# Optimization experiments

Measured on AMD Instinct MI355X. Metric: run time of the kernel, lower is better.

The kernel has to match this reference:

```python
import jax, jax.numpy as jnp
import numpy as np

N_ITER = 9      # n_iter in entmax_nsect_cuda(X, alpha=1.5, n_iter=9, n_sections=4)
N_SECTIONS = 4  # quaternary section search


def _entmax15_nsect(X):
    """1.5-entmax via n-section threshold search.

    p = [(alpha-1)*x - tau]_+^(1/(alpha-1)) with alpha=1.5 -> p = relu(x/2 - tau)^2,
    tau chosen so sum_j p_j = 1. tau lies in [max(x/2)-1, max(x/2)]; the interval is
    narrowed by N_SECTIONS-section search for N_ITER iterations (f is decreasing in tau).
    """
    Xs = X * 0.5
    mx = jnp.max(Xs, axis=-1, keepdims=True)      # (n, 1)
    lo = mx - 1.0
    hi = mx

    def f(tau):  # sum relu(x - tau)^2 - 1, decreasing in tau; (n, 1)
        return jnp.sum(jnp.square(jnp.maximum(Xs - tau, 0.0)), axis=-1, keepdims=True) - 1.0

    for _ in range(N_ITER):
        width = (hi - lo) / N_SECTIONS
        # count of interior grid points with f >= 0 gives the bracketing section index
        count = jnp.zeros_like(lo)
        for j in range(1, N_SECTIONS):
            count = count + (f(lo + j * width) >= 0.0).astype(Xs.dtype)
        lo = lo + width * count
        hi = lo + width

    tau = 0.5 * (lo + hi)
    p = jnp.square(jnp.maximum(Xs - tau, 0.0))
    return p / jnp.sum(p, axis=-1, keepdims=True)  # exact renormalization of approx projection


def setup_inputs() -> dict:
    key = jax.random.key(0)
    kx, kt = jax.random.split(key)
    n, c = 4096, 32000
    X = jax.random.normal(kx, (n, c), dtype=jnp.float32)
    target = jax.random.randint(kt, (n,), 0, c, dtype=jnp.int64)
    return {"X": X, "target": target}


def reference(X, target):
    n = X.shape[0]
    p = _entmax15_nsect(X)                                   # (n, C) simplex projection
    # omega (Tsallis entropy term for alpha=1.5): (1 - sum p^{1.5}) / 0.75
    omega = (1.0 - jnp.sum(p * jnp.sqrt(p), axis=-1)) / 0.75
    # p_star <- p - e_target  (scatter_add_ of -1 at the target column)
    p_star = p.at[jnp.arange(n), target].add(-1.0)
    loss = omega + jnp.sum(p_star * X, axis=-1)              # + einsum('ij,ij->i', p_star, X)
    # ignore_index = -100 < 0 -> no masking; reduction = 'elementwise_mean'
    return jnp.sum(loss) / n
```

## Files before the change

### kernel.cpp

```cpp
#include <hip/hip_runtime.h>


#define NITER 9
#define TGRAW 1.5f
#define CAPW  320
#define EXCAP 3072
#define NW    16

__device__ __forceinline__ float wave_max_f(float m) {
    #pragma unroll
    for (int off = 32; off > 0; off >>= 1) m = fmaxf(m, __shfl_xor(m, off));
    return m;
}
__device__ __forceinline__ float wave_sum_f(float s) {
    #pragma unroll
    for (int off = 32; off > 0; off >>= 1) s += __shfl_xor(s, off);
    return s;
}

__global__ __launch_bounds__(1024, 8)
void entmax_loss_kernel(const float* __restrict__ X,
                        const int* __restrict__ target,
                        float* __restrict__ row_loss, int c) {
    const int r    = blockIdx.x;
    const int tid  = threadIdx.x;
    const int w    = tid >> 6;
    const int lane = tid & 63;
    const float* __restrict__ Xr = X + (size_t)r * (size_t)c;

    __shared__ float seg[NW][CAPW];
    __shared__ int   segcnt[NW];
    __shared__ float s_red[NW];
    __shared__ int   s_excnt[NW];
    __shared__ float ex[EXCAP];
    __shared__ float s_r3[3][NW];
    __shared__ int   s_flag;
    __shared__ int   s_tg;
    __shared__ float s_xtg;

    if (tid == 0) {
        s_flag = 0;
        const int tg = target[r];
        s_tg = tg;
        s_xtg = Xr[tg];
    }

    const int c4 = c >> 2;
    const unsigned long long lt = (1ull << lane) - 1ull;
    float* __restrict__ segw = seg[w];
    float m = -3e38f;
    int   cnt = 0;
    for (int b = 0; b < 2; ++b) {
        float4 v[4];
        #pragma unroll
        for (int k = 0; k < 4; ++k) {
            const int i4 = tid + (b * 4 + k) * 1024;
            if (i4 < c4) v[k] = ((const float4*)Xr)[i4];
            else { v[k].x = v[k].y = v[k].z = v[k].w = -3e38f; }
        }
        #pragma unroll
        for (int k = 0; k < 4; ++k) {
            m = fmaxf(m, fmaxf(fmaxf(v[k].x, v[k].y), fmaxf(v[k].z, v[k].w)));
            const float e[4] = {v[k].x, v[k].y, v[k].z, v[k].w};
            #pragma unroll
            for (int j = 0; j < 4; ++j) {
                const bool p = e[j] > TGRAW;
                const unsigned long long bl = __ballot(p);
                const int pos = cnt + (int)__popcll(bl & lt);
                if (p && pos < CAPW) segw[pos] = e[j];
                cnt += (int)__popcll(bl);
            }
        }
    }
    m = wave_max_f(m);
    if (lane == 0) {
        s_red[w] = m;
        segcnt[w] = cnt;
        if (cnt > CAPW) s_flag = 1;
    }
    __syncthreads();

    float rm = s_red[0];
    #pragma unroll
    for (int i = 1; i < NW; ++i) rm = fmaxf(rm, s_red[i]);
    const bool fb = (s_flag != 0) || (rm < TGRAW + 2.0f);

    if (!fb) {
        const float thr = rm - 2.0f;
        const int sc = segcnt[w];
        int ec = 0;
        for (int i0 = 0; i0 < sc; i0 += 64) {
            const int i = i0 + lane;
            const bool p = (i < sc) && (segw[i] > thr);
            ec += (int)__popcll(__ballot(p));
        }
        if (lane == 0) s_excnt[w] = ec;
        __syncthreads();

        int off = 0, total = 0;
        #pragma unroll
        for (int u = 0; u < NW; ++u) {
            const int e = s_excnt[u];
            if (u < w) off += e;
            total += e;
        }
        if (total <= EXCAP) {
            int pos = off;
            for (int i0 = 0; i0 < sc; i0 += 64) {
                const int i = i0 + lane;
                const bool p = (i < sc) && (segw[i] > thr);
                const unsigned long long bl = __ballot(p);
                if (p) ex[pos + (int)__popcll(bl & lt)] = 0.5f * segw[i];
                pos += (int)__popcll(bl);
            }
            __syncthreads();
            if (w == 0) {
                float lo = 0.5f * rm - 1.0f, hi = 0.5f * rm;
                for (int it = 0; it < NITER; ++it) {
                    const float w4 = (hi - lo) * 0.25f;
                    const float t1 = lo + w4, t2 = lo + 2.f * w4, t3 = lo + 3.f * w4;
                    float f1 = 0.f, f2 = 0.f, f3 = 0.f;
                    for (int i = lane; i < total; i += 64) {
                        const float x = ex[i];
                        float d;
                        d = fmaxf(x - t1, 0.f); f1 = fmaf(d, d, f1);
                        d = fmaxf(x - t2, 0.f); f2 = fmaf(d, d, f2);
                        d = fmaxf(x - t3, 0.f); f3 = fmaf(d, d, f3);
                    }
                    f1 = wave_sum_f(f1); f2 = wave_sum_f(f2); f3 = wave_sum_f(f3);
                    const int cc = (f1 >= 1.f) + (f2 >= 1.f) + (f3 >= 1.f);
                    lo += w4 * (float)cc;
                    hi = lo + w4;
                }
                const float tau = 0.5f * (lo + hi);
                float S1 = 0.f, SX = 0.f, S3 = 0.f;
                for (int i = lane; i < total; i += 64) {
                    const float x = ex[i];
                    const float d = fmaxf(x - tau, 0.f), q = d * d;
                    S1 += q; SX = fmaf(q, x, SX); S3 = fmaf(q, d, S3);
                }
                S1 = wave_sum_f(S1); SX = wave_sum_f(SX); S3 = wave_sum_f(S3);
                if (lane == 0) {
                    const float omega = (1.f - S3 / (S1 * sqrtf(S1))) * (4.f / 3.f);
                    row_loss[r] = omega + 2.f * SX / S1 - s_xtg;
                }
            }
            return;
        }
    }

    {
        float lo = 0.5f * rm - 1.0f, hi = 0.5f * rm;
        for (int it = 0; it < NITER; ++it) {
            const float w4 = (hi - lo) * 0.25f;
            const float t1 = lo + w4, t2 = lo + 2.f * w4, t3 = lo + 3.f * w4;
            float f1 = 0.f, f2 = 0.f, f3 = 0.f;
            for (int i = tid; i < c; i += 1024) {
                const float x = 0.5f * Xr[i];
                float d;
                d = fmaxf(x - t1, 0.f); f1 = fmaf(d, d, f1);
                d = fmaxf(x - t2, 0.f); f2 = fmaf(d, d, f2);
                d = fmaxf(x - t3, 0.f); f3 = fmaf(d, d, f3);
            }
            f1 = wave_sum_f(f1); f2 = wave_sum_f(f2); f3 = wave_sum_f(f3);
            __syncthreads();
            if (lane == 0) { s_r3[0][w] = f1; s_r3[1][w] = f2; s_r3[2][w] = f3; }
            __syncthreads();
            float a = 0.f, bb = 0.f, g = 0.f;
            #pragma unroll
            for (int u = 0; u < NW; ++u) { a += s_r3[0][u]; bb += s_r3[1][u]; g += s_r3[2][u]; }
            const int cc = (a >= 1.f) + (bb >= 1.f) + (g >= 1.f);
            lo += w4 * (float)cc;
            hi = lo + w4;
        }
        const float tau = 0.5f * (lo + hi);
        float S1 = 0.f, SX = 0.f, S3 = 0.f;
        for (int i = tid; i < c; i += 1024) {
            const float x = 0.5f * Xr[i];
            const float d = fmaxf(x - tau, 0.f), q = d * d;
            S1 += q; SX = fmaf(q, x, SX); S3 = fmaf(q, d, S3);
        }
        S1 = wave_sum_f(S1); SX = wave_sum_f(SX); S3 = wave_sum_f(S3);
        __syncthreads();
        if (lane == 0) { s_r3[0][w] = S1; s_r3[1][w] = SX; s_r3[2][w] = S3; }
        __syncthreads();
        if (tid == 0) {
            float a = 0.f, bb = 0.f, g = 0.f;
            #pragma unroll
            for (int u = 0; u < NW; ++u) { a += s_r3[0][u]; bb += s_r3[1][u]; g += s_r3[2][u]; }
            const float omega = (1.f - g / (a * sqrtf(a))) * (4.f / 3.f);
            row_loss[r] = omega + 2.f * bb / a - s_xtg;
        }
    }
}

__global__ __launch_bounds__(256, 4)
void fallback_kernel(const float* __restrict__ X, const int* __restrict__ target,
                     float* __restrict__ row_loss, int n, int c) {
    const int wv   = threadIdx.x >> 6;
    const int lane = threadIdx.x & 63;
    const int r = blockIdx.x * 4 + wv;
    if (r >= n) return;
    const float* __restrict__ Xr = X + (size_t)r * (size_t)c;
    float m = -3e38f;
    for (int i = lane; i < c; i += 64) m = fmaxf(m, Xr[i]);
    m = wave_max_f(m);
    float lo = 0.5f * m - 1.0f, hi = 0.5f * m;
    for (int it = 0; it < NITER; ++it) {
        const float w4 = (hi - lo) * 0.25f;
        const float t1 = lo + w4, t2 = lo + 2.f * w4, t3 = lo + 3.f * w4;
        float f1 = 0.f, f2 = 0.f, f3 = 0.f;
        for (int i = lane; i < c; i += 64) {
            const float x = 0.5f * Xr[i];
            float d;
            d = fmaxf(x - t1, 0.f); f1 = fmaf(d, d, f1);
            d = fmaxf(x - t2, 0.f); f2 = fmaf(d, d, f2);
            d = fmaxf(x - t3, 0.f); f3 = fmaf(d, d, f3);
        }
        f1 = wave_sum_f(f1); f2 = wave_sum_f(f2); f3 = wave_sum_f(f3);
        const int cc = (f1 >= 1.f) + (f2 >= 1.f) + (f3 >= 1.f);
        lo += w4 * (float)cc;
        hi = lo + w4;
    }
    const float tau = 0.5f * (lo + hi);
    float S1 = 0.f, SX = 0.f, S3 = 0.f;
    for (int i = lane; i < c; i += 64) {
        const float x = 0.5f * Xr[i];
        const float d = fmaxf(x - tau, 0.f), q = d * d;
        S1 += q; SX = fmaf(q, x, SX); S3 = fmaf(q, d, S3);
    }
    S1 = wave_sum_f(S1); SX = wave_sum_f(SX); S3 = wave_sum_f(S3);
    if (lane == 0) {
        const float omega = (1.f - S3 / (S1 * sqrtf(S1))) * (4.f / 3.f);
        row_loss[r] = omega + 2.f * SX / S1 - Xr[target[r]];
    }
}

__global__ __launch_bounds__(1024)
void reduce_mean_kernel(const float* __restrict__ vv, float* __restrict__ out, int n) {
    __shared__ float s_red[16];
    float s = 0.f;
    for (int i = threadIdx.x; i < n; i += 1024) s += vv[i];
    s = wave_sum_f(s);
    const int wv = threadIdx.x >> 6;
    const int lane = threadIdx.x & 63;
    if (lane == 0) s_red[wv] = s;
    __syncthreads();
    if (threadIdx.x == 0) {
        float t = 0.f;
        for (int i = 0; i < 16; ++i) t += s_red[i];
        out[0] = t / (float)n;
    }
}

extern "C" void kernel_launch(void* const* d_in, const int* in_sizes, int n_in,
                              void* d_out, int out_size, void* d_ws, size_t ws_size,
                              hipStream_t stream) {
    (void)n_in; (void)out_size;
    const float* X      = (const float*)d_in[0];
    const int*   target = (const int*)d_in[1];
    float*       out    = (float*)d_out;
    float*       row_loss = (float*)d_ws;

    const int n = in_sizes[1];
    const int c = in_sizes[0] / n;

    const bool fast = ((c & 3) == 0) && (c <= 32768) &&
                      (ws_size >= (size_t)n * sizeof(float));
    if (fast) {
        entmax_loss_kernel<<<n, 1024, 0, stream>>>(X, target, row_loss, c);
    } else {
        fallback_kernel<<<(n + 3) / 4, 256, 0, stream>>>(X, target, row_loss, n, c);
    }
    reduce_mean_kernel<<<1, 1024, 0, stream>>>(row_loss, out, n);
}
```

Baseline: 162.5 us.

## Halve block size, prefetch row chunks, and spread threshold search across all waves

The row kernel drops from 1024 to 512 threads per row. Each thread now covers four chunks of float4 loads, and the next chunk is register-prefetched while the current one is filtered, which overlaps memory latency with the ballot compaction. The n-section search over the compacted candidates previously ran on wave 0 alone and now runs on all 8 waves. A double-buffered shared partial array keeps it to one barrier per iteration. The per-wave candidate capacity grows to 512 so the larger per-wave slice does not overflow. This adds barriers and register pressure in exchange for fewer idle waves and better latency hiding.

```diff
diff --git a/kernel.cpp b/kernel.cpp
--- a/kernel.cpp
+++ b/kernel.cpp
@@ -2,10 +2,11 @@
 
 
 #define NITER 9
+#define NTHR  512
+#define NWAVE 8
 #define TGRAW 1.5f
-#define CAPW  320
+#define CAPW  512
 #define EXCAP 3072
-#define NW    16
 
 __device__ __forceinline__ float wave_max_f(float m) {
     #pragma unroll
@@ -18,7 +19,7 @@
     return s;
 }
 
-__global__ __launch_bounds__(1024, 8)
+__global__ __launch_bounds__(NTHR, 8)
 void entmax_loss_kernel(const float* __restrict__ X,
                         const int* __restrict__ target,
                         float* __restrict__ row_loss, int c) {
@@ -28,40 +29,45 @@
     const int lane = tid & 63;
     const float* __restrict__ Xr = X + (size_t)r * (size_t)c;
 
-    __shared__ float seg[NW][CAPW];
-    __shared__ int   segcnt[NW];
-    __shared__ float s_red[NW];
-    __shared__ int   s_excnt[NW];
+    __shared__ float seg[NWAVE][CAPW];
+    __shared__ int   segcnt[NWAVE];
+    __shared__ float s_red[NWAVE];
+    __shared__ int   s_excnt[NWAVE];
     __shared__ float ex[EXCAP];
-    __shared__ float s_r3[3][NW];
+    __shared__ float s_part[2][3][NWAVE];
+    __shared__ float s_fin[3][NWAVE];
     __shared__ int   s_flag;
-    __shared__ int   s_tg;
     __shared__ float s_xtg;
 
-    if (tid == 0) {
-        s_flag = 0;
-        const int tg = target[r];
-        s_tg = tg;
-        s_xtg = Xr[tg];
-    }
+    if (tid == 0) { s_flag = 0; s_xtg = Xr[target[r]]; }
 
     const int c4 = c >> 2;
     const unsigned long long lt = (1ull << lane) - 1ull;
     float* __restrict__ segw = seg[w];
     float m = -3e38f;
     int   cnt = 0;
-    for (int b = 0; b < 2; ++b) {
-        float4 v[4];
+
+    float4 cur[4], nxt[4];
+    #pragma unroll
+    for (int k = 0; k < 4; ++k) {
+        const int i4 = tid + k * NTHR;
+        if (i4 < c4) cur[k] = ((const float4*)Xr)[i4];
+        else { cur[k].x = cur[k].y = cur[k].z = cur[k].w = -3e38f; }
+    }
+    #pragma unroll
+    for (int b = 0; b < 4; ++b) {
+        if (b < 3) {
+            #pragma unroll
+            for (int k = 0; k < 4; ++k) {
+                const int i4 = tid + ((b + 1) * 4 + k) * NTHR;
+                if (i4 < c4) nxt[k] = ((const float4*)Xr)[i4];
+                else { nxt[k].x = nxt[k].y = nxt[k].z = nxt[k].w = -3e38f; }
+            }
+        }
         #pragma unroll
         for (int k = 0; k < 4; ++k) {
-            const int i4 = tid + (b * 4 + k) * 1024;
-            if (i4 < c4) v[k] = ((const float4*)Xr)[i4];
-            else { v[k].x = v[k].y = v[k].z = v[k].w = -3e38f; }
-        }
-        #pragma unroll
-        for (int k = 0; k < 4; ++k) {
-            m = fmaxf(m, fmaxf(fmaxf(v[k].x, v[k].y), fmaxf(v[k].z, v[k].w)));
-            const float e[4] = {v[k].x, v[k].y, v[k].z, v[k].w};
+            const float e[4] = {cur[k].x, cur[k].y, cur[k].z, cur[k].w};
+            m = fmaxf(m, fmaxf(fmaxf(e[0], e[1]), fmaxf(e[2], e[3])));
             #pragma unroll
             for (int j = 0; j < 4; ++j) {
                 const bool p = e[j] > TGRAW;
@@ -71,6 +77,10 @@
                 cnt += (int)__popcll(bl);
             }
         }
+        if (b < 3) {
+            #pragma unroll
+            for (int k = 0; k < 4; ++k) cur[k] = nxt[k];
+        }
     }
     m = wave_max_f(m);
     if (lane == 0) {
@@ -82,7 +92,7 @@
 
     float rm = s_red[0];
     #pragma unroll
-    for (int i = 1; i < NW; ++i) rm = fmaxf(rm, s_red[i]);
+    for (int i = 1; i < NWAVE; ++i) rm = fmaxf(rm, s_red[i]);
     const bool fb = (s_flag != 0) || (rm < TGRAW + 2.0f);
 
     if (!fb) {
@@ -99,7 +109,7 @@
 
         int off = 0, total = 0;
         #pragma unroll
-        for (int u = 0; u < NW; ++u) {
+        for (int u = 0; u < NWAVE; ++u) {
             const int e = s_excnt[u];
             if (u < w) off += e;
             total += e;
@@ -114,36 +124,51 @@
                 pos += (int)__popcll(bl);
             }
             __syncthreads();
-            if (w == 0) {
-                float lo = 0.5f * rm - 1.0f, hi = 0.5f * rm;
-                for (int it = 0; it < NITER; ++it) {
-                    const float w4 = (hi - lo) * 0.25f;
-                    const float t1 = lo + w4, t2 = lo + 2.f * w4, t3 = lo + 3.f * w4;
-                    float f1 = 0.f, f2 = 0.f, f3 = 0.f;
-                    for (int i = lane; i < total; i += 64) {
-                        const float x = ex[i];
-                        float d;
-                        d = fmaxf(x - t1, 0.f); f1 = fmaf(d, d, f1);
-                        d = fmaxf(x - t2, 0.f); f2 = fmaf(d, d, f2);
-                        d = fmaxf(x - t3, 0.f); f3 = fmaf(d, d, f3);
-                    }
-                    f1 = wave_sum_f(f1); f2 = wave_sum_f(f2); f3 = wave_sum_f(f3);
-                    const int cc = (f1 >= 1.f) + (f2 >= 1.f) + (f3 >= 1.f);
-                    lo += w4 * (float)cc;
-                    hi = lo + w4;
+            float lo = 0.5f * rm - 1.0f, hi = 0.5f * rm;
+            for (int it = 0; it < NITER; ++it) {
+                const float w4 = (hi - lo) * 0.25f;
+                const float t1 = lo + w4, t2 = lo + 2.f * w4, t3 = lo + 3.f * w4;
+                float f1 = 0.f, f2 = 0.f, f3 = 0.f;
+                for (int i = tid; i < total; i += NTHR) {
+                    const float x = ex[i];
+                    float d;
+                    d = fmaxf(x - t1, 0.f); f1 = fmaf(d, d, f1);
+                    d = fmaxf(x - t2, 0.f); f2 = fmaf(d, d, f2);
+                    d = fmaxf(x - t3, 0.f); f3 = fmaf(d, d, f3);
                 }
-                const float tau = 0.5f * (lo + hi);
-                float S1 = 0.f, SX = 0.f, S3 = 0.f;
-                for (int i = lane; i < total; i += 64) {
-                    const float x = ex[i];
-                    const float d = fmaxf(x - tau, 0.f), q = d * d;
-                    S1 += q; SX = fmaf(q, x, SX); S3 = fmaf(q, d, S3);
+                f1 = wave_sum_f(f1); f2 = wave_sum_f(f2); f3 = wave_sum_f(f3);
+                const int pb = it & 1;
+                if (lane == 0) {
+                    s_part[pb][0][w] = f1; s_part[pb][1][w] = f2; s_part[pb][2][w] = f3;
                 }
-                S1 = wave_sum_f(S1); SX = wave_sum_f(SX); S3 = wave_sum_f(S3);
-                if (lane == 0) {
-                    const float omega = (1.f - S3 / (S1 * sqrtf(S1))) * (4.f / 3.f);
-                    row_loss[r] = omega + 2.f * SX / S1 - s_xtg;
+                __syncthreads();
+                float a = 0.f, bb = 0.f, g = 0.f;
+                #pragma unroll
+                for (int u = 0; u < NWAVE; ++u) {
+                    a += s_part[pb][0][u]; bb += s_part[pb][1][u]; g += s_part[pb][2][u];
                 }
+                const int cc = (a >= 1.f) + (bb >= 1.f) + (g >= 1.f);
+                lo += w4 * (float)cc;
+                hi = lo + w4;
+            }
+            const float tau = 0.5f * (lo + hi);
+            float S1 = 0.f, SX = 0.f, S3 = 0.f;
+            for (int i = tid; i < total; i += NTHR) {
+                const float x = ex[i];
+                const float d = fmaxf(x - tau, 0.f), q = d * d;
+                S1 += q; SX = fmaf(q, x, SX); S3 = fmaf(q, d, S3);
+            }
+            S1 = wave_sum_f(S1); SX = wave_sum_f(SX); S3 = wave_sum_f(S3);
+            if (lane == 0) { s_fin[0][w] = S1; s_fin[1][w] = SX; s_fin[2][w] = S3; }
+            __syncthreads();
+            if (tid == 0) {
+                float a = 0.f, bb = 0.f, g = 0.f;
+                #pragma unroll
+                for (int u = 0; u < NWAVE; ++u) {
+                    a += s_fin[0][u]; bb += s_fin[1][u]; g += s_fin[2][u];
+                }
+                const float omega = (1.f - g / (a * sqrtf(a))) * (4.f / 3.f);
+                row_loss[r] = omega + 2.f * bb / a - s_xtg;
             }
             return;
         }
@@ -155,7 +180,7 @@
             const float w4 = (hi - lo) * 0.25f;
             const float t1 = lo + w4, t2 = lo + 2.f * w4, t3 = lo + 3.f * w4;
             float f1 = 0.f, f2 = 0.f, f3 = 0.f;
-            for (int i = tid; i < c; i += 1024) {
+            for (int i = tid; i < c; i += NTHR) {
                 const float x = 0.5f * Xr[i];
                 float d;
                 d = fmaxf(x - t1, 0.f); f1 = fmaf(d, d, f1);
@@ -164,30 +189,34 @@
             }
             f1 = wave_sum_f(f1); f2 = wave_sum_f(f2); f3 = wave_sum_f(f3);
             __syncthreads();
-            if (lane == 0) { s_r3[0][w] = f1; s_r3[1][w] = f2; s_r3[2][w] = f3; }
+            if (lane == 0) { s_fin[0][w] = f1; s_fin[1][w] = f2; s_fin[2][w] = f3; }
             __syncthreads();
             float a = 0.f, bb = 0.f, g = 0.f;
             #pragma unroll
-            for (int u = 0; u < NW; ++u) { a += s_r3[0][u]; bb += s_r3[1][u]; g += s_r3[2][u]; }
+            for (int u = 0; u < NWAVE; ++u) {
+                a += s_fin[0][u]; bb += s_fin[1][u]; g += s_fin[2][u];
+            }
             const int cc = (a >= 1.f) + (bb >= 1.f) + (g >= 1.f);
             lo += w4 * (float)cc;
             hi = lo + w4;
         }
         const float tau = 0.5f * (lo + hi);
         float S1 = 0.f, SX = 0.f, S3 = 0.f;
-        for (int i = tid; i < c; i += 1024) {
+        for (int i = tid; i < c; i += NTHR) {
             const float x = 0.5f * Xr[i];
             const float d = fmaxf(x - tau, 0.f), q = d * d;
             S1 += q; SX = fmaf(q, x, SX); S3 = fmaf(q, d, S3);
         }
         S1 = wave_sum_f(S1); SX = wave_sum_f(SX); S3 = wave_sum_f(S3);
         __syncthreads();
-        if (lane == 0) { s_r3[0][w] = S1; s_r3[1][w] = SX; s_r3[2][w] = S3; }
+        if (lane == 0) { s_fin[0][w] = S1; s_fin[1][w] = SX; s_fin[2][w] = S3; }
         __syncthreads();
         if (tid == 0) {
             float a = 0.f, bb = 0.f, g = 0.f;
             #pragma unroll
-            for (int u = 0; u < NW; ++u) { a += s_r3[0][u]; bb += s_r3[1][u]; g += s_r3[2][u]; }
+            for (int u = 0; u < NWAVE; ++u) {
+                a += s_fin[0][u]; bb += s_fin[1][u]; g += s_fin[2][u];
+            }
             const float omega = (1.f - g / (a * sqrtf(a))) * (4.f / 3.f);
             row_loss[r] = omega + 2.f * bb / a - s_xtg;
         }
@@ -268,7 +297,7 @@
     const bool fast = ((c & 3) == 0) && (c <= 32768) &&
                       (ws_size >= (size_t)n * sizeof(float));
     if (fast) {
-        entmax_loss_kernel<<<n, 1024, 0, stream>>>(X, target, row_loss, c);
+        entmax_loss_kernel<<<n, NTHR, 0, stream>>>(X, target, row_loss, c);
     } else {
         fallback_kernel<<<(n + 3) / 4, 256, 0, stream>>>(X, target, row_loss, n, c);
     }
```

Result: slower. 213.8 us (+31.5%).
